# Kernel optimization log

Measured on AMD Instinct MI355X. Metric: run time of the kernel, lower is better.

Reference implementation:

```python
import jax, jax.numpy as jnp
import numpy as np

N = 20000          # num nodes
E = 250000         # num edges
B = 128            # num graphs in batch
Fin = 512
Fqk = 512
Fv = 512
H = 8              # nheads


def setup_inputs() -> dict:
    key = jax.random.key(0)
    k1, k2, k3, k4 = jax.random.split(key, 4)
    x = jax.random.normal(k1, (N, Fin), dtype=jnp.float32)
    batch = jnp.sort(jax.random.randint(k2, (N,), 0, B)).astype(jnp.int32)
    ei = jax.random.randint(k3, (2, E), 0, N).astype(jnp.int32)
    # proj weight of Linear(Fin, 2*Fqk+Fv, bias=False); stored as (Fin, Ftot)
    W = (jax.random.normal(k4, (Fin, 2 * Fqk + Fv), dtype=jnp.float32)
         / np.sqrt(Fin).astype(np.float32))
    return {"x": x, "batch": batch, "ei": ei, "W": W}


def reference(x, batch, ei, W):
    src, dest = ei[0], ei[1]
    n = x.shape[0]
    Fh = Fqk // H            # head dim for q/k
    Fhv = Fv // H            # head dim for v
    scaling = float(Fh) ** (-0.5)

    qkv = x @ W                                    # (N, 2*Fqk+Fv)
    q, k, v = jnp.split(qkv, [Fqk, 2 * Fqk], axis=-1)
    q = (q * scaling).reshape(n, H, Fh)
    k = k.reshape(n, H, Fh)
    v = v.reshape(n, H, Fhv)

    # edge-wise gathers
    qs = q[src]                                    # (E, H, Fh)
    ks = k[dest]                                   # (E, H, Fh)
    vs = v[dest]                                   # (E, H, Fhv)

    # per-edge, per-head attention scores
    aw = jnp.einsum('ehf,ehf->eh', qs, ks)         # (E, H)

    # segment softmax over edges sharing the same src node (stable)
    m = jax.ops.segment_max(aw, src, num_segments=n)       # (N, H)
    e = jnp.exp(aw - m[src])                                # (E, H)
    denom = jax.ops.segment_sum(e, src, num_segments=n)     # (N, H)
    alpha = e / denom[src]                                   # (E, H)

    # scatter-weighted aggregation of values back to src nodes
    out = jax.ops.segment_sum(alpha[:, :, None] * vs, src, num_segments=n)  # (N, H, Fhv)
    return out.reshape(n, Fv)
```

## Files before the change

### kernel.cpp

```cpp
#include <hip/hip_runtime.h>
#include <cstdint>

typedef float f32x4 __attribute__((ext_vector_type(4)));
typedef __bf16 bf16x8 __attribute__((ext_vector_type(8)));

__device__ __forceinline__ unsigned short f2b(float f) {
  unsigned int u = __float_as_uint(f);
  u = (u + 0x7fffu + ((u >> 16) & 1u)) >> 16;
  return (unsigned short)u;
}

__device__ __forceinline__ void unpack8(uint4 u, float* f) {
  f[0] = __uint_as_float((u.x & 0xffffu) << 16);
  f[1] = __uint_as_float(u.x & 0xffff0000u);
  f[2] = __uint_as_float((u.y & 0xffffu) << 16);
  f[3] = __uint_as_float(u.y & 0xffff0000u);
  f[4] = __uint_as_float((u.z & 0xffffu) << 16);
  f[5] = __uint_as_float(u.z & 0xffff0000u);
  f[6] = __uint_as_float((u.w & 0xffffu) << 16);
  f[7] = __uint_as_float(u.w & 0xffff0000u);
}

__device__ __forceinline__ void async_copy16(const void* g, void* l) {
  __builtin_amdgcn_global_load_lds(
      (const __attribute__((address_space(1))) void*)g,
      (__attribute__((address_space(3))) void*)l, 16, 0, 0);
}

__global__ __launch_bounds__(256) void prep_kernel(
    const float* __restrict__ x, unsigned short* __restrict__ xb,
    int nrows, int mpad, int fin,
    const float* __restrict__ W, unsigned short* __restrict__ Wt, int NT,
    const int* __restrict__ src, const int* __restrict__ dst,
    int* __restrict__ deg, int* __restrict__ edst, int E,
    int nbConvx, int nbConvw) {
  __shared__ float tile[32][33];
  int bx = blockIdx.x, t = threadIdx.x;

  if (bx < nbConvx) {
    int i8 = bx * 256 + t;
    int total = mpad * fin / 8;
    if (i8 >= total) return;
    int row = (i8 * 8) / fin;
    unsigned short o[8];
    if (row < nrows) {
      const float4* p = (const float4*)(x + (size_t)i8 * 8);
      float4 a = p[0], b = p[1];
      o[0] = f2b(a.x); o[1] = f2b(a.y); o[2] = f2b(a.z); o[3] = f2b(a.w);
      o[4] = f2b(b.x); o[5] = f2b(b.y); o[6] = f2b(b.z); o[7] = f2b(b.w);
    } else {
#pragma unroll
      for (int j = 0; j < 8; ++j) o[j] = 0;
    }
    uint4 w;
    w.x = (unsigned int)o[0] | ((unsigned int)o[1] << 16);
    w.y = (unsigned int)o[2] | ((unsigned int)o[3] << 16);
    w.z = (unsigned int)o[4] | ((unsigned int)o[5] << 16);
    w.w = (unsigned int)o[6] | ((unsigned int)o[7] << 16);
    *(uint4*)(xb + (size_t)i8 * 8) = w;
  } else if (bx < nbConvx + nbConvw) {
    int b = bx - nbConvx;
    int tilesPerRow = NT / 32;
    int n0 = (b % tilesPerRow) * 32, k0 = (b / tilesPerRow) * 32;
    int r = t >> 5, c = t & 31;
#pragma unroll
    for (int ph = 0; ph < 4; ++ph)
      tile[r + 8 * ph][c] = W[(size_t)(k0 + r + 8 * ph) * NT + n0 + c];
    __syncthreads();
#pragma unroll
    for (int ph = 0; ph < 4; ++ph) {
      int rr = r + 8 * ph;
      int nn = n0 + rr;
      float s = (nn < 512) ? 0.125f : 1.0f;
      Wt[(size_t)nn * 512 + k0 + c] = f2b(tile[c][rr] * s);
    }
  } else {
    int e = (bx - nbConvx - nbConvw) * 256 + t;
    if (e < E) {
      int s = src[e], d = dst[e];
      int j = atomicAdd(&deg[s], 1);
      if (j < 64) edst[(size_t)s * 64 + j] = d;
    }
  }
}

__global__ __launch_bounds__(1024, 4) void gemm256_kernel(
    const unsigned short* __restrict__ A, const unsigned short* __restrict__ Bt,
    unsigned short* __restrict__ C, int K, int NT, int NPAN) {
  __shared__ __align__(16) unsigned short SM[49152];

  int bx = blockIdx.x, tid = threadIdx.x;
  int nwg = gridDim.x;
  int q8 = nwg >> 3, r8 = nwg & 7;
  int xcd = bx & 7, idx = bx >> 3;
  int wgid = (xcd < r8 ? xcd * (q8 + 1) : r8 * (q8 + 1) + (xcd - r8) * q8) + idx;
  int mtile = wgid / NPAN, npanel = wgid % NPAN;
  int m0 = mtile * 256, n0 = npanel * 256;

  int wave = tid >> 6, lane = tid & 63;
  int wm = wave >> 2, wn = wave & 3;
  int hi = lane >> 4, l15 = lane & 15;

  int srow = (tid >> 6) * 16 + l15;
  int scol = ((tid >> 4) & 3) * 8;
  const unsigned short* pA = A + (size_t)(m0 + srow) * K + scol;
  const unsigned short* pB = Bt + (size_t)(n0 + srow) * K + scol;

  async_copy16(pA, SM + tid * 8);
  async_copy16(pB, SM + 24576 + tid * 8);
  async_copy16(pA + 32, SM + 8192 + tid * 8);
  async_copy16(pB + 32, SM + 24576 + 8192 + tid * 8);
  asm volatile("s_waitcnt vmcnt(2)" ::: "memory");
  __builtin_amdgcn_s_barrier();
  __builtin_amdgcn_sched_barrier(0);

  f32x4 acc[4][4] = {};
  int aoff = wm * 2048 + lane * 8;
  int boff = 24576 + wn * 2048 + lane * 8;

#pragma unroll
  for (int t = 0; t < 16; ++t) {
    int sb = (t % 3) * 8192;
    bf16x8 av[4], bv[4];
    const unsigned short* a_ = SM + sb + aoff;
    const unsigned short* b_ = SM + sb + boff;
#pragma unroll
    for (int i = 0; i < 4; ++i) av[i] = *(const bf16x8*)(a_ + i * 512);
#pragma unroll
    for (int j = 0; j < 4; ++j) bv[j] = *(const bf16x8*)(b_ + j * 512);
    if (t + 2 < 16) {
      int s2 = ((t + 2) % 3) * 8192;
      async_copy16(pA + (t + 2) * 32, SM + s2 + tid * 8);
      async_copy16(pB + (t + 2) * 32, SM + 24576 + s2 + tid * 8);
    }
    asm volatile("s_waitcnt lgkmcnt(0)" ::: "memory");
    __builtin_amdgcn_sched_barrier(0);
    __builtin_amdgcn_s_setprio(1);
#pragma unroll
    for (int i = 0; i < 4; ++i)
#pragma unroll
      for (int j = 0; j < 4; ++j)
        acc[i][j] = __builtin_amdgcn_mfma_f32_16x16x32_bf16(av[i], bv[j], acc[i][j], 0, 0, 0);
    __builtin_amdgcn_s_setprio(0);
    if (t + 2 < 16) {
      asm volatile("s_waitcnt vmcnt(2)" ::: "memory");
    } else {
      asm volatile("s_waitcnt vmcnt(0)" ::: "memory");
    }
    __builtin_amdgcn_sched_barrier(0);
    __builtin_amdgcn_s_barrier();
    __builtin_amdgcn_sched_barrier(0);
  }

  __syncthreads();
  unsigned short* cs = SM + wave * 640;
  unsigned short* gC = C + (size_t)(m0 + wm * 64) * NT + n0 + wn * 64;
  int erow = lane >> 2, echunk = (lane & 3) * 8;
#pragma unroll
  for (int i = 0; i < 4; ++i)
#pragma unroll
    for (int p = 0; p < 2; ++p) {
#pragma unroll
      for (int jj = 0; jj < 2; ++jj)
#pragma unroll
        for (int q = 0; q < 4; ++q)
          cs[(hi * 4 + q) * 40 + jj * 16 + l15] = f2b(acc[i][2 * p + jj][q]);
      uint4 val = *(const uint4*)&cs[erow * 40 + echunk];
      *(uint4*)&gC[(size_t)(i * 16 + erow) * NT + p * 32 + echunk] = val;
    }
}

__global__ __launch_bounds__(256) void attn_kernel(
    const unsigned short* __restrict__ qkv, const int* __restrict__ deg,
    const int* __restrict__ edst, float* __restrict__ out, int n) {
  int wave = threadIdx.x >> 6, lane = threadIdx.x & 63;
  int node = blockIdx.x * 4 + wave;
  if (node >= n) return;

  float q[8];
  unpack8(*(const uint4*)(qkv + (size_t)node * 1536 + lane * 8), q);

  float acc[8] = {0.f, 0.f, 0.f, 0.f, 0.f, 0.f, 0.f, 0.f};
  float l = 0.f;
  int dn = deg[node];
  if (dn > 64) dn = 64;
  int beg = node * 64, end = beg + dn;

  int i = beg;
  for (; i + 4 <= end; i += 4) {
    int d0 = edst[i], d1 = edst[i + 1], d2 = edst[i + 2], d3 = edst[i + 3];
    const uint4* p0 = (const uint4*)(qkv + (size_t)d0 * 1536 + 512 + lane * 8);
    const uint4* p1 = (const uint4*)(qkv + (size_t)d1 * 1536 + 512 + lane * 8);
    const uint4* p2 = (const uint4*)(qkv + (size_t)d2 * 1536 + 512 + lane * 8);
    const uint4* p3 = (const uint4*)(qkv + (size_t)d3 * 1536 + 512 + lane * 8);
    uint4 kr0 = p0[0], vr0 = p0[64];
    uint4 kr1 = p1[0], vr1 = p1[64];
    uint4 kr2 = p2[0], vr2 = p2[64];
    uint4 kr3 = p3[0], vr3 = p3[64];
#pragma unroll
    for (int u = 0; u < 4; ++u) {
      uint4 kv = (u == 0) ? kr0 : (u == 1) ? kr1 : (u == 2) ? kr2 : kr3;
      uint4 vv = (u == 0) ? vr0 : (u == 1) ? vr1 : (u == 2) ? vr2 : vr3;
      float kf[8], vf[8];
      unpack8(kv, kf);
      unpack8(vv, vf);
      float part = 0.f;
#pragma unroll
      for (int j = 0; j < 8; ++j) part = fmaf(q[j], kf[j], part);
      part += __shfl_xor(part, 1);
      part += __shfl_xor(part, 2);
      part += __shfl_xor(part, 4);
      float p = __expf(part);
      l += p;
#pragma unroll
      for (int j = 0; j < 8; ++j) acc[j] = fmaf(p, vf[j], acc[j]);
    }
  }
  for (; i < end; ++i) {
    int d = edst[i];
    const uint4* pp = (const uint4*)(qkv + (size_t)d * 1536 + 512 + lane * 8);
    uint4 kv = pp[0], vv = pp[64];
    float kf[8], vf[8];
    unpack8(kv, kf);
    unpack8(vv, vf);
    float part = 0.f;
#pragma unroll
    for (int j = 0; j < 8; ++j) part = fmaf(q[j], kf[j], part);
    part += __shfl_xor(part, 1);
    part += __shfl_xor(part, 2);
    part += __shfl_xor(part, 4);
    float p = __expf(part);
    l += p;
#pragma unroll
    for (int j = 0; j < 8; ++j) acc[j] = fmaf(p, vf[j], acc[j]);
  }

  float inv = (l > 0.f) ? 1.f / l : 0.f;
  float4 o0, o1;
  o0.x = acc[0] * inv; o0.y = acc[1] * inv; o0.z = acc[2] * inv; o0.w = acc[3] * inv;
  o1.x = acc[4] * inv; o1.y = acc[5] * inv; o1.z = acc[6] * inv; o1.w = acc[7] * inv;
  float4* op = (float4*)(out + (size_t)node * 512 + lane * 8);
  op[0] = o0;
  op[1] = o1;
}

extern "C" void kernel_launch(void* const* d_in, const int* in_sizes, int n_in,
                              void* d_out, int out_size, void* d_ws, size_t ws_size,
                              hipStream_t stream) {
  const float* x = (const float*)d_in[0];
  const int* ei = (const int*)d_in[2];
  const float* W = (const float*)d_in[3];
  float* out = (float*)d_out;

  const int N = in_sizes[1];
  const int E = in_sizes[2] / 2;
  const int Fin = in_sizes[0] / N;
  const int FT = in_sizes[3] / Fin;
  const int MPAD = ((N + 255) / 256) * 256;

  const int* src = ei;
  const int* dst = ei + E;

  char* ws = (char*)d_ws;
  size_t off = 0;
  auto alloc = [&](size_t bytes) {
    void* p = ws + off;
    off = (off + bytes + 255) & ~(size_t)255;
    return p;
  };
  unsigned short* xb  = (unsigned short*)alloc((size_t)MPAD * Fin * 2);
  unsigned short* Wt  = (unsigned short*)alloc((size_t)FT * Fin * 2);
  unsigned short* qkv = (unsigned short*)alloc((size_t)MPAD * FT * 2);
  int* deg  = (int*)alloc((size_t)N * 4);
  int* edst = (int*)alloc((size_t)N * 64 * 4);

  hipMemsetAsync(deg, 0, (size_t)N * 4, stream);

  int nbConvx = (MPAD * Fin / 8 + 255) / 256;
  int nbConvw = (FT / 32) * (Fin / 32);
  int nbBucket = (E + 255) / 256;
  prep_kernel<<<nbConvx + nbConvw + nbBucket, 256, 0, stream>>>(
      x, xb, N, MPAD, Fin, W, Wt, FT, src, dst, deg, edst, E, nbConvx, nbConvw);

  int NPAN = FT / 256;
  int MTILES = MPAD / 256;
  gemm256_kernel<<<MTILES * NPAN, 1024, 0, stream>>>(xb, Wt, qkv, Fin, FT, NPAN);

  attn_kernel<<<(N + 3) / 4, 256, 0, stream>>>(qkv, deg, edst, out, N);
}
```

Baseline: 156.1 us.

## Fuse fp32-to-bf16 conversion of x into GEMM A-tile loading

Removes the separate prep pass that converts x to a bf16 buffer. The GEMM now loads fp32 rows of x into registers, converts them to bf16 and writes them to LDS, prefetching one step ahead, while B still uses async global-to-LDS copies. This saves writing and re-reading a bf16 copy of x, but the GEMM now reads twice as many A bytes, and each A block is read by 6 N-panels. The register-staged path also adds conversion ALU work and register pressure inside the main loop.

```diff
diff --git a/kernel.cpp b/kernel.cpp
--- a/kernel.cpp
+++ b/kernel.cpp
@@ -28,38 +28,14 @@
 }
 
 __global__ __launch_bounds__(256) void prep_kernel(
-    const float* __restrict__ x, unsigned short* __restrict__ xb,
-    int nrows, int mpad, int fin,
     const float* __restrict__ W, unsigned short* __restrict__ Wt, int NT,
     const int* __restrict__ src, const int* __restrict__ dst,
-    int* __restrict__ deg, int* __restrict__ edst, int E,
-    int nbConvx, int nbConvw) {
+    int* __restrict__ deg, int* __restrict__ edst, int E, int nbConvw) {
   __shared__ float tile[32][33];
   int bx = blockIdx.x, t = threadIdx.x;
 
-  if (bx < nbConvx) {
-    int i8 = bx * 256 + t;
-    int total = mpad * fin / 8;
-    if (i8 >= total) return;
-    int row = (i8 * 8) / fin;
-    unsigned short o[8];
-    if (row < nrows) {
-      const float4* p = (const float4*)(x + (size_t)i8 * 8);
-      float4 a = p[0], b = p[1];
-      o[0] = f2b(a.x); o[1] = f2b(a.y); o[2] = f2b(a.z); o[3] = f2b(a.w);
-      o[4] = f2b(b.x); o[5] = f2b(b.y); o[6] = f2b(b.z); o[7] = f2b(b.w);
-    } else {
-#pragma unroll
-      for (int j = 0; j < 8; ++j) o[j] = 0;
-    }
-    uint4 w;
-    w.x = (unsigned int)o[0] | ((unsigned int)o[1] << 16);
-    w.y = (unsigned int)o[2] | ((unsigned int)o[3] << 16);
-    w.z = (unsigned int)o[4] | ((unsigned int)o[5] << 16);
-    w.w = (unsigned int)o[6] | ((unsigned int)o[7] << 16);
-    *(uint4*)(xb + (size_t)i8 * 8) = w;
-  } else if (bx < nbConvx + nbConvw) {
-    int b = bx - nbConvx;
+  if (bx < nbConvw) {
+    int b = bx;
     int tilesPerRow = NT / 32;
     int n0 = (b % tilesPerRow) * 32, k0 = (b / tilesPerRow) * 32;
     int r = t >> 5, c = t & 31;
@@ -75,7 +51,7 @@
       Wt[(size_t)nn * 512 + k0 + c] = f2b(tile[c][rr] * s);
     }
   } else {
-    int e = (bx - nbConvx - nbConvw) * 256 + t;
+    int e = (bx - nbConvw) * 256 + t;
     if (e < E) {
       int s = src[e], d = dst[e];
       int j = atomicAdd(&deg[s], 1);
@@ -85,8 +61,8 @@
 }
 
 __global__ __launch_bounds__(1024, 4) void gemm256_kernel(
-    const unsigned short* __restrict__ A, const unsigned short* __restrict__ Bt,
-    unsigned short* __restrict__ C, int K, int NT, int NPAN) {
+    const float* __restrict__ X, const unsigned short* __restrict__ Bt,
+    unsigned short* __restrict__ C, int K, int NT, int NPAN, int nrows) {
   __shared__ __align__(16) unsigned short SM[49152];
 
   int bx = blockIdx.x, tid = threadIdx.x;
@@ -103,14 +79,37 @@
 
   int srow = (tid >> 6) * 16 + l15;
   int scol = ((tid >> 4) & 3) * 8;
-  const unsigned short* pA = A + (size_t)(m0 + srow) * K + scol;
+  bool inb = (m0 + srow) < nrows;
+  const float* pX = X + (size_t)(m0 + srow) * K + scol;
   const unsigned short* pB = Bt + (size_t)(n0 + srow) * K + scol;
 
-  async_copy16(pA, SM + tid * 8);
+  auto loadA = [&](int t, float4& f0, float4& f1) {
+    if (inb) {
+      f0 = *(const float4*)(pX + t * 32);
+      f1 = *(const float4*)(pX + t * 32 + 4);
+    } else {
+      f0 = make_float4(0.f, 0.f, 0.f, 0.f);
+      f1 = make_float4(0.f, 0.f, 0.f, 0.f);
+    }
+  };
+  auto cvtWriteA = [&](const float4& f0, const float4& f1, int slot) {
+    uint4 w;
+    w.x = (unsigned)f2b(f0.x) | ((unsigned)f2b(f0.y) << 16);
+    w.y = (unsigned)f2b(f0.z) | ((unsigned)f2b(f0.w) << 16);
+    w.z = (unsigned)f2b(f1.x) | ((unsigned)f2b(f1.y) << 16);
+    w.w = (unsigned)f2b(f1.z) | ((unsigned)f2b(f1.w) << 16);
+    *(uint4*)(SM + slot * 8192 + tid * 8) = w;
+  };
+
   async_copy16(pB, SM + 24576 + tid * 8);
-  async_copy16(pA + 32, SM + 8192 + tid * 8);
   async_copy16(pB + 32, SM + 24576 + 8192 + tid * 8);
-  asm volatile("s_waitcnt vmcnt(2)" ::: "memory");
+  __builtin_amdgcn_sched_barrier(0);
+  float4 f00, f01, nf0, nf1;
+  loadA(0, f00, f01);
+  loadA(1, nf0, nf1);
+  __builtin_amdgcn_sched_barrier(0);
+  cvtWriteA(f00, f01, 0);
+  asm volatile("s_waitcnt lgkmcnt(0)" ::: "memory");
   __builtin_amdgcn_s_barrier();
   __builtin_amdgcn_sched_barrier(0);
 
@@ -130,11 +129,10 @@
     for (int j = 0; j < 4; ++j) bv[j] = *(const bf16x8*)(b_ + j * 512);
     if (t + 2 < 16) {
       int s2 = ((t + 2) % 3) * 8192;
-      async_copy16(pA + (t + 2) * 32, SM + s2 + tid * 8);
       async_copy16(pB + (t + 2) * 32, SM + 24576 + s2 + tid * 8);
     }
-    asm volatile("s_waitcnt lgkmcnt(0)" ::: "memory");
-    __builtin_amdgcn_sched_barrier(0);
+    if (t + 1 < 16) cvtWriteA(nf0, nf1, (t + 1) % 3);
+    if (t + 2 < 16) loadA(t + 2, nf0, nf1);
     __builtin_amdgcn_s_setprio(1);
 #pragma unroll
     for (int i = 0; i < 4; ++i)
@@ -147,6 +145,7 @@
     } else {
       asm volatile("s_waitcnt vmcnt(0)" ::: "memory");
     }
+    asm volatile("s_waitcnt lgkmcnt(0)" ::: "memory");
     __builtin_amdgcn_sched_barrier(0);
     __builtin_amdgcn_s_barrier();
     __builtin_amdgcn_sched_barrier(0);
@@ -268,7 +267,6 @@
     off = (off + bytes + 255) & ~(size_t)255;
     return p;
   };
-  unsigned short* xb  = (unsigned short*)alloc((size_t)MPAD * Fin * 2);
   unsigned short* Wt  = (unsigned short*)alloc((size_t)FT * Fin * 2);
   unsigned short* qkv = (unsigned short*)alloc((size_t)MPAD * FT * 2);
   int* deg  = (int*)alloc((size_t)N * 4);
@@ -276,15 +274,14 @@
 
   hipMemsetAsync(deg, 0, (size_t)N * 4, stream);
 
-  int nbConvx = (MPAD * Fin / 8 + 255) / 256;
   int nbConvw = (FT / 32) * (Fin / 32);
   int nbBucket = (E + 255) / 256;
-  prep_kernel<<<nbConvx + nbConvw + nbBucket, 256, 0, stream>>>(
-      x, xb, N, MPAD, Fin, W, Wt, FT, src, dst, deg, edst, E, nbConvx, nbConvw);
+  prep_kernel<<<nbConvw + nbBucket, 256, 0, stream>>>(
+      W, Wt, FT, src, dst, deg, edst, E, nbConvw);
 
   int NPAN = FT / 256;
   int MTILES = MPAD / 256;
-  gemm256_kernel<<<MTILES * NPAN, 1024, 0, stream>>>(xb, Wt, qkv, Fin, FT, NPAN);
+  gemm256_kernel<<<MTILES * NPAN, 1024, 0, stream>>>(x, Wt, qkv, Fin, FT, NPAN, N);
 
   attn_kernel<<<(N + 3) / 4, 256, 0, stream>>>(qkv, deg, edst, out, N);
 }
```

New measurement: 155.7 us. About the same (-0.3%).
